# Kernel tuning notes

Measured on AMD Instinct MI355X. Metric: run time of the kernel, lower is better.

The kernel has to match this reference:

```python
import jax, jax.numpy as jnp
from jax import lax
import numpy as np

B, T, U, V = 8, 200, 50, 1024  # acts label axis is U+1
BLANK = 0


def setup_inputs() -> dict:
    key = jax.random.key(0)
    k1, k2, k3, k4 = jax.random.split(key, 4)
    acts = jax.random.normal(k1, (B, T, U + 1, V), dtype=jnp.float32)
    labels = jax.random.randint(k2, (B, U), 1, V)          # non-blank targets
    act_lens = jax.random.randint(k3, (B,), T // 2, T + 1).astype(jnp.int32)
    label_lens = jax.random.randint(k4, (B,), U // 2, U + 1).astype(jnp.int32)
    return {"acts": acts, "labels": labels, "act_lens": act_lens, "label_lens": label_lens}


def _rnnt_loss(acts, labels, act_lens, label_lens):
    # acts: (B,T,U+1,V) raw logits -> log-softmax over vocab
    logp = jax.nn.log_softmax(acts, axis=-1)
    lp_blank = logp[..., BLANK]                                   # (B,T,U+1)
    idx = labels[:, None, :, None]                                # (B,1,U,1) broadcasts over T
    lp_emit = jnp.take_along_axis(logp[:, :, :U, :], idx, axis=-1)[..., 0]  # (B,T,U)

    # alpha[t,u] = logaddexp(alpha[t-1,u]+blank(t-1,u), alpha[t,u-1]+emit(t,u-1))
    # row t=0: pure emissions along u
    alpha0 = jnp.concatenate(
        [jnp.zeros((B, 1), logp.dtype), jnp.cumsum(lp_emit[:, 0, :], axis=1)], axis=1
    )  # (B,U+1)

    def t_step(prev_row, inp):
        blank_prev, emit_t = inp                 # (B,U+1), (B,U)
        from_top = prev_row + blank_prev         # contribution from t-1
        def u_step(c, xs):                       # serial left-to-right in u
            ft, em = xs                          # (B,), (B,)
            c = jnp.logaddexp(ft, c + em)
            return c, c
        c0 = from_top[:, 0]
        _, rest = lax.scan(u_step, c0, (from_top[:, 1:].T, emit_t.T))  # (U,B)
        new_row = jnp.concatenate([c0[:, None], rest.T], axis=1)       # (B,U+1)
        return new_row, new_row

    blank_rows = jnp.swapaxes(lp_blank, 0, 1)    # (T,B,U+1)
    emit_rows = jnp.swapaxes(lp_emit, 0, 1)      # (T,B,U)
    _, later_rows = lax.scan(t_step, alpha0, (blank_rows[:-1], emit_rows[1:]))
    alphas = jnp.concatenate([alpha0[None], later_rows], axis=0)       # (T,B,U+1)

    b = jnp.arange(B)
    tl = act_lens - 1
    ul = label_lens
    log_like = alphas[tl, b, ul] + lp_blank[b, tl, ul]  # final blank emission
    return -jnp.sum(log_like)  # size_average=False -> summed cost


def reference(acts, labels, act_lens, label_lens):
    return _rnnt_loss(acts, labels, act_lens, label_lens)
```

## Files before the change

### kernel.cpp

```cpp
#include <hip/hip_runtime.h>
#include <math.h>

#define BB 8
#define TT 200
#define UU 50
#define VV 1024
#define U1 (UU + 1)
#define NROWS (BB * TT * U1)

#define LOG2E 1.44269504088896340736f
#define LN2   0.69314718055994530942f

typedef float f4v __attribute__((ext_vector_type(4)));

__device__ __forceinline__ float wave_shr1(float x) {
    int xi = __builtin_bit_cast(int, x);
    int r  = __builtin_amdgcn_update_dpp(0, xi, 0x138, 0xF, 0xF, true);
    return __builtin_bit_cast(float, r);
}

__global__ __launch_bounds__(256) void k_logp(const float* __restrict__ acts,
                                              const int* __restrict__ labels,
                                              float* __restrict__ lpb,
                                              float* __restrict__ lpe,
                                              float* __restrict__ out) {
    if (blockIdx.x == 0 && threadIdx.x == 0) out[0] = 0.0f;
    const int wave = threadIdx.x >> 6;
    const int lane = threadIdx.x & 63;
    const int row  = blockIdx.x * 4 + wave;

    int b   = row / (TT * U1);
    int rem = row - b * (TT * U1);
    int t   = rem / U1;
    int u   = rem - t * U1;
    int lab = (u < UU) ? labels[b * UU + u] : 0;

    const f4v* p = (const f4v*)(acts + (size_t)row * VV);
    f4v v0 = __builtin_nontemporal_load(p + lane);
    f4v v1 = __builtin_nontemporal_load(p + 64 + lane);
    f4v v2 = __builtin_nontemporal_load(p + 128 + lane);
    f4v v3 = __builtin_nontemporal_load(p + 192 + lane);

    const int cidx = lab >> 8, lidx = (lab >> 2) & 63, eidx = lab & 3;
    float alab = 0.0f;

    float sum = __expf(v0.x) + __expf(v0.y) + __expf(v0.z) + __expf(v0.w);
    if (cidx == 0) alab = (eidx & 2) ? ((eidx & 1) ? v0.w : v0.z) : ((eidx & 1) ? v0.y : v0.x);
    sum += __expf(v1.x) + __expf(v1.y) + __expf(v1.z) + __expf(v1.w);
    if (cidx == 1) alab = (eidx & 2) ? ((eidx & 1) ? v1.w : v1.z) : ((eidx & 1) ? v1.y : v1.x);
    sum += __expf(v2.x) + __expf(v2.y) + __expf(v2.z) + __expf(v2.w);
    if (cidx == 2) alab = (eidx & 2) ? ((eidx & 1) ? v2.w : v2.z) : ((eidx & 1) ? v2.y : v2.x);
    sum += __expf(v3.x) + __expf(v3.y) + __expf(v3.z) + __expf(v3.w);
    if (cidx == 3) alab = (eidx & 2) ? ((eidx & 1) ? v3.w : v3.z) : ((eidx & 1) ? v3.y : v3.x);

#pragma unroll
    for (int s = 1; s < 64; s <<= 1) sum += __shfl_xor(sum, s, 64);

    float logZ = __logf(sum);
    if (u < UU && lane == lidx) lpe[(b * TT + t) * UU + u] = alab - logZ;
    if (lane == 0)              lpb[row] = v0.x - logZ;
}

__global__ __launch_bounds__(256) void k_dp(const float* __restrict__ lpb,
                                            const float* __restrict__ lpe,
                                            const int* __restrict__ act_lens,
                                            const int* __restrict__ label_lens,
                                            float* __restrict__ out) {
    __shared__ __align__(16) float s_lpb[TT * U1];
    __shared__ __align__(16) float s_lpe[TT * UU];

    const int b = blockIdx.x;
    const float4* gb4 = (const float4*)(lpb + (size_t)b * TT * U1);
    const float4* ge4 = (const float4*)(lpe + (size_t)b * TT * UU);
    float4* sb4 = (float4*)s_lpb;
    float4* se4 = (float4*)s_lpe;
    for (int i = threadIdx.x; i < TT * U1 / 4; i += 256) {
        float4 v = gb4[i];
        v.x *= LOG2E; v.y *= LOG2E; v.z *= LOG2E; v.w *= LOG2E;
        sb4[i] = v;
    }
    for (int i = threadIdx.x; i < TT * UU / 4; i += 256) {
        float4 v = ge4[i];
        v.x *= LOG2E; v.y *= LOG2E; v.z *= LOG2E; v.w *= LOG2E;
        se4[i] = v;
    }
    __syncthreads();
    if (threadIdx.x >= 64) return;

    const int u  = threadIdx.x;
    const int uc = min(u, UU);
    const int tl = act_lens[b] - 1;
    const int ul = label_lens[b];
    const int dtgt = tl + ul;
    const float NEG = -INFINITY;
    const float bsave = s_lpb[tl * U1 + ul];

    float Aprev = (u == 0) ? 0.0f : NEG;
    float saved = (dtgt == 0 && u == 0) ? bsave : NEG;

#pragma unroll 5
    for (int d = 1; d <= TT - 1 + UU; ++d) {
        float Aup = wave_shr1(Aprev);
        int t  = d - u;
        int tb = min(max(t - 1, 0), TT - 1);
        int te = min(max(t, 0), TT - 1);
        float bv = s_lpb[tb * U1 + uc];
        float ev = s_lpe[te * UU + max(uc - 1, 0)];
        bool cellok = (t >= 0) & (t < TT) & (u <= UU);
        float ft = (cellok & (t >= 1)) ? Aprev + bv : NEG;
        float em = (cellok & (u >= 1)) ? Aup + ev   : NEG;
        float mm = fmaxf(ft, em);
        float dd = fminf(ft, em) - mm;
        float A  = mm + __builtin_amdgcn_logf(1.0f + __builtin_amdgcn_exp2f(dd));
        A = cellok ? A : NEG;
        saved = (d == dtgt && u == ul) ? A + bsave : saved;
        Aprev = A;
    }
    if (u == ul) atomicAdd(out, -(saved * LN2));
}

extern "C" void kernel_launch(void* const* d_in, const int* in_sizes, int n_in,
                              void* d_out, int out_size, void* d_ws, size_t ws_size,
                              hipStream_t stream) {
    const float* acts       = (const float*)d_in[0];
    const int*   labels     = (const int*)d_in[1];
    const int*   act_lens   = (const int*)d_in[2];
    const int*   label_lens = (const int*)d_in[3];

    float* ws  = (float*)d_ws;
    float* lpb = ws;
    float* lpe = lpb + NROWS;
    float* out = (float*)d_out;

    k_logp<<<NROWS / 4, 256, 0, stream>>>(acts, labels, lpb, lpe, out);
    k_dp<<<BB, 256, 0, stream>>>(lpb, lpe, act_lens, label_lens, out);
}
```

Measured before the change: 75.52 us.

## Double-buffer log-softmax rows via global_load_lds and end DP at target diagonal

Each wave now handles four rows. The next row is prefetched into LDS with global_load_lds while the current row's log-sum-exp is computed, so memory latency overlaps with math. Launching fewer blocks also cuts per-block overhead. Separately, the DP diagonal loop stops at the target diagonal instead of running to the maximum, skipping wasted serial iterations. The risks are the extra LDS use per block, which may limit occupancy, and the hand-written vmcnt waits, which must match the real number of outstanding loads.

Result: slower. 86.88 us (+15.0%).

```diff
diff --git a/kernel.cpp b/kernel.cpp
--- a/kernel.cpp
+++ b/kernel.cpp
@@ -7,11 +7,10 @@
 #define VV 1024
 #define U1 (UU + 1)
 #define NROWS (BB * TT * U1)
+#define RPW 4
 
 #define LOG2E 1.44269504088896340736f
 #define LN2   0.69314718055994530942f
-
-typedef float f4v __attribute__((ext_vector_type(4)));
 
 __device__ __forceinline__ float wave_shr1(float x) {
     int xi = __builtin_bit_cast(int, x);
@@ -25,40 +24,74 @@
                                               float* __restrict__ lpe,
                                               float* __restrict__ out) {
     if (blockIdx.x == 0 && threadIdx.x == 0) out[0] = 0.0f;
+    __shared__ __align__(16) float s_buf[4 * 2 * VV];
     const int wave = threadIdx.x >> 6;
     const int lane = threadIdx.x & 63;
-    const int row  = blockIdx.x * 4 + wave;
+    const int row0 = (blockIdx.x * 4 + wave) * RPW;
+    float* sl[2] = { &s_buf[wave * 2 * VV], &s_buf[wave * 2 * VV + VV] };
 
-    int b   = row / (TT * U1);
-    int rem = row - b * (TT * U1);
-    int t   = rem / U1;
-    int u   = rem - t * U1;
-    int lab = (u < UU) ? labels[b * UU + u] : 0;
+    int labA[RPW], uA[RPW], idxA[RPW];
+#pragma unroll
+    for (int k = 0; k < RPW; ++k) {
+        int r = row0 + k;
+        int b = r / (TT * U1), rem = r - b * (TT * U1);
+        int t = rem / U1, u = rem - t * U1;
+        uA[k]   = u;
+        labA[k] = (u < UU) ? labels[b * UU + u] : 0;
+        idxA[k] = (b * TT + t) * UU + u;
+    }
 
-    const f4v* p = (const f4v*)(acts + (size_t)row * VV);
-    f4v v0 = __builtin_nontemporal_load(p + lane);
-    f4v v1 = __builtin_nontemporal_load(p + 64 + lane);
-    f4v v2 = __builtin_nontemporal_load(p + 128 + lane);
-    f4v v3 = __builtin_nontemporal_load(p + 192 + lane);
-
-    const int cidx = lab >> 8, lidx = (lab >> 2) & 63, eidx = lab & 3;
-    float alab = 0.0f;
-
-    float sum = __expf(v0.x) + __expf(v0.y) + __expf(v0.z) + __expf(v0.w);
-    if (cidx == 0) alab = (eidx & 2) ? ((eidx & 1) ? v0.w : v0.z) : ((eidx & 1) ? v0.y : v0.x);
-    sum += __expf(v1.x) + __expf(v1.y) + __expf(v1.z) + __expf(v1.w);
-    if (cidx == 1) alab = (eidx & 2) ? ((eidx & 1) ? v1.w : v1.z) : ((eidx & 1) ? v1.y : v1.x);
-    sum += __expf(v2.x) + __expf(v2.y) + __expf(v2.z) + __expf(v2.w);
-    if (cidx == 2) alab = (eidx & 2) ? ((eidx & 1) ? v2.w : v2.z) : ((eidx & 1) ? v2.y : v2.x);
-    sum += __expf(v3.x) + __expf(v3.y) + __expf(v3.z) + __expf(v3.w);
-    if (cidx == 3) alab = (eidx & 2) ? ((eidx & 1) ? v3.w : v3.z) : ((eidx & 1) ? v3.y : v3.x);
+    {
+        const float* g = acts + (size_t)row0 * VV;
+        __builtin_amdgcn_sched_barrier(0);
+#pragma unroll
+        for (int c = 0; c < 4; ++c)
+            __builtin_amdgcn_global_load_lds(g + c * 256 + lane * 4, sl[0] + c * 256, 16, 0, 0);
+        __builtin_amdgcn_sched_barrier(0);
+    }
 
 #pragma unroll
-    for (int s = 1; s < 64; s <<= 1) sum += __shfl_xor(sum, s, 64);
+    for (int k = 0; k < RPW; ++k) {
+        const int row = row0 + k;
+        float* cur = sl[k & 1];
+        if (k < RPW - 1) {
+            const float* g = acts + (size_t)(row + 1) * VV;
+            float* nxt = sl[(k + 1) & 1];
+            __builtin_amdgcn_sched_barrier(0);
+#pragma unroll
+            for (int c = 0; c < 4; ++c)
+                __builtin_amdgcn_global_load_lds(g + c * 256 + lane * 4, nxt + c * 256, 16, 0, 0);
+            __builtin_amdgcn_sched_barrier(0);
+            asm volatile("s_waitcnt vmcnt(4)" ::: "memory");
+        } else {
+            asm volatile("s_waitcnt vmcnt(0)" ::: "memory");
+        }
 
-    float logZ = __logf(sum);
-    if (u < UU && lane == lidx) lpe[(b * TT + t) * UU + u] = alab - logZ;
-    if (lane == 0)              lpb[row] = v0.x - logZ;
+        float4 v0 = *(const float4*)(cur + 0 * 256 + lane * 4);
+        float4 v1 = *(const float4*)(cur + 1 * 256 + lane * 4);
+        float4 v2 = *(const float4*)(cur + 2 * 256 + lane * 4);
+        float4 v3 = *(const float4*)(cur + 3 * 256 + lane * 4);
+
+        const int lab = labA[k];
+        const int cidx = lab >> 8, lidx = (lab >> 2) & 63, eidx = lab & 3;
+        float alab = 0.0f;
+
+        float sum = __expf(v0.x) + __expf(v0.y) + __expf(v0.z) + __expf(v0.w);
+        if (cidx == 0) alab = (eidx & 2) ? ((eidx & 1) ? v0.w : v0.z) : ((eidx & 1) ? v0.y : v0.x);
+        sum += __expf(v1.x) + __expf(v1.y) + __expf(v1.z) + __expf(v1.w);
+        if (cidx == 1) alab = (eidx & 2) ? ((eidx & 1) ? v1.w : v1.z) : ((eidx & 1) ? v1.y : v1.x);
+        sum += __expf(v2.x) + __expf(v2.y) + __expf(v2.z) + __expf(v2.w);
+        if (cidx == 2) alab = (eidx & 2) ? ((eidx & 1) ? v2.w : v2.z) : ((eidx & 1) ? v2.y : v2.x);
+        sum += __expf(v3.x) + __expf(v3.y) + __expf(v3.z) + __expf(v3.w);
+        if (cidx == 3) alab = (eidx & 2) ? ((eidx & 1) ? v3.w : v3.z) : ((eidx & 1) ? v3.y : v3.x);
+
+#pragma unroll
+        for (int s = 1; s < 64; s <<= 1) sum += __shfl_xor(sum, s, 64);
+        float logZ = __logf(sum);
+
+        if (uA[k] < UU && lane == lidx) lpe[idxA[k]] = alab - logZ;
+        if (lane == 0)                  lpb[row]    = v0.x - logZ;
+    }
 }
 
 __global__ __launch_bounds__(256) void k_dp(const float* __restrict__ lpb,
@@ -99,7 +132,7 @@
     float saved = (dtgt == 0 && u == 0) ? bsave : NEG;
 
 #pragma unroll 5
-    for (int d = 1; d <= TT - 1 + UU; ++d) {
+    for (int d = 1; d <= dtgt; ++d) {
         float Aup = wave_shr1(Aprev);
         int t  = d - u;
         int tb = min(max(t - 1, 0), TT - 1);
@@ -132,6 +165,6 @@
     float* lpe = lpb + NROWS;
     float* out = (float*)d_out;
 
-    k_logp<<<NROWS / 4, 256, 0, stream>>>(acts, labels, lpb, lpe, out);
+    k_logp<<<NROWS / (4 * RPW), 256, 0, stream>>>(acts, labels, lpb, lpe, out);
     k_dp<<<BB, 256, 0, stream>>>(lpb, lpe, act_lens, label_lens, out);
 }
```
